# Performance work log

Measured on AMD Instinct MI355X. Metric: run time of the kernel, lower is better.

The kernel has to match this reference:

```python
import jax, jax.numpy as jnp
import numpy as np

B, L, D_IN, D = 64, 512, 1024, 1024


def setup_inputs() -> dict:
    key = jax.random.key(0)
    k1, k2, k3, k4, k5 = jax.random.split(key, 5)
    x = jax.random.normal(k1, (B, L, D_IN), dtype=jnp.float32)
    Wk = jax.random.normal(k2, (D_IN, 3 * D), dtype=jnp.float32) * (1.0 / np.sqrt(D_IN))
    Wr = jax.random.normal(k3, (D, 3 * D), dtype=jnp.float32) * (1.0 / np.sqrt(D))
    c0 = jax.random.normal(k4, (B, D), dtype=jnp.float32)
    h0 = jax.random.normal(k5, (B, D), dtype=jnp.float32)
    return {"x": x, "Wk": Wk, "Wr": Wr, "c0": c0, "h0": h0}


def reference(x, Wk, Wr, c0, h0):
    # Precompute input projection as one large GEMM: [B,L,3D]
    x_proj = jnp.einsum("bli,ig->blg", x, Wk)

    def step(carry, xp_t):
        c, h = carry  # c: long-term memory [B,D], h: previous output [B,D]
        gates = xp_t + h @ Wr  # [B,3D]
        f, o, g = jnp.split(gates, 3, axis=-1)
        sf = jax.nn.sigmoid(f)
        c_new = c * sf + (1.0 - sf) * jnp.tanh(g)
        h_new = jax.nn.sigmoid(o) * jnp.tanh(c_new)
        return (c_new, h_new), h_new

    # scan over time: move L to leading axis
    _, hs = jax.lax.scan(step, (c0, h0), jnp.swapaxes(x_proj, 0, 1))
    return jnp.swapaxes(hs, 0, 1)  # [B,L,D]
```

## Files before the change

### kernel.cpp

```cpp
#include <hip/hip_runtime.h>


typedef float    f32x4 __attribute__((ext_vector_type(4)));
typedef _Float16 half8 __attribute__((ext_vector_type(8)));
typedef _Float16 half4 __attribute__((ext_vector_type(4)));

#define AS1 __attribute__((address_space(1)))
#define AS3 __attribute__((address_space(3)))

#define B_  64
#define L_  512
#define D_  1024
#define N3_ 3072

#define WKT_OFF   0LL
#define WRT_OFF   6291456LL
#define XH_OFF    12582912LL
#define H16_OFF   79691776LL
#define BAR_OFF   79953920LL
#define XPROJ_OFF 79958016LL

__device__ __forceinline__ float sigmoidf_fast(float x) {
  return __builtin_amdgcn_rcpf(1.f + __builtin_amdgcn_exp2f(-1.4426950408889634f * x));
}
__device__ __forceinline__ float tanhf_fast(float x) {
  return 1.f - 2.f * __builtin_amdgcn_rcpf(1.f + __builtin_amdgcn_exp2f(2.8853900817779268f * x));
}

#define ALOAD(dst, addr) \
  asm volatile("global_load_dwordx4 %0, %1, off" : "=v"(dst) : "v"(addr))
#define VMCNT0() asm volatile("s_waitcnt vmcnt(0)" ::: "memory")

__device__ __forceinline__ void gload_lds16(const void* g, void* l) {
  __builtin_amdgcn_global_load_lds((const AS1 unsigned int*)g,
                                   (AS3 unsigned int*)l, 16, 0, 0);
}

__global__ void zero_bar(unsigned* __restrict__ bar) {
  bar[blockIdx.x * 256 + threadIdx.x] = 0u;
}

__global__ __launch_bounds__(256) void transpose_f16(
    const float* __restrict__ Wk, const float* __restrict__ Wr,
    _Float16* __restrict__ WkT, _Float16* __restrict__ WrT)
{
  __shared__ float tile[32][33];
  int b = blockIdx.x;
  const float* in = Wk; _Float16* outp = WkT;
  if (b >= 3072) { b -= 3072; in = Wr; outp = WrT; }
  const int n0 = (b % 96) * 32;
  const int k0 = (b / 96) * 32;
  const int tx = threadIdx.x & 31, ty = threadIdx.x >> 5;
#pragma unroll
  for (int i = 0; i < 32; i += 8)
    tile[ty + i][tx] = in[(size_t)(k0 + ty + i) * N3_ + n0 + tx];
  __syncthreads();
#pragma unroll
  for (int i = 0; i < 32; i += 8)
    outp[(size_t)(n0 + ty + i) * D_ + k0 + tx] = (_Float16)tile[tx][ty + i];
}

__global__ void convert_inputs(const f32x4* __restrict__ x, const f32x4* __restrict__ h0,
                               half4* __restrict__ xh, half4* __restrict__ h16a,
                               half4* __restrict__ h16b)
{
  const int NX = (B_ * L_ * D_) / 4;
  const int NH = (B_ * D_) / 4;
  for (int i = blockIdx.x * blockDim.x + threadIdx.x; i < NX + NH;
       i += gridDim.x * blockDim.x) {
    if (i < NX) {
      xh[i] = __builtin_convertvector(x[i], half4);
    } else {
      half4 v = __builtin_convertvector(h0[i - NX], half4);
      h16a[i - NX] = v;
      h16b[i - NX] = v;
    }
  }
}

__global__ __launch_bounds__(256) void gemm_xproj(
    const _Float16* __restrict__ A,
    const _Float16* __restrict__ BT,
    _Float16* __restrict__ C)
{
  __shared__ _Float16 As[128 * 32];
  __shared__ _Float16 Bs[128 * 32];
  const int tid = threadIdx.x, wave = tid >> 6, lane = tid & 63;
  const int mt = blockIdx.x / 24, ntile = blockIdx.x % 24;
  const int m0 = mt * 128, n0 = ntile * 128;
  const int l15 = lane & 15, l4h = lane >> 4;
  const int wm = (wave >> 1) * 64, wn = (wave & 1) * 64;

  const int c0i = wave * 2;
  const int lrow = lane >> 2;
  const int skel = 8 * ((lane & 3) ^ (lrow & 3));

  f32x4 acc[4][4];
#pragma unroll
  for (int i = 0; i < 4; ++i)
#pragma unroll
    for (int j = 0; j < 4; ++j) { f32x4 z = {0.f,0.f,0.f,0.f}; acc[i][j] = z; }

  for (int kk = 0; kk < 32; ++kk) {
    __syncthreads();
#pragma unroll
    for (int i = 0; i < 2; ++i) {
      const int c = c0i + i;
      const int row = c * 16 + lrow;
      gload_lds16(A  + (((size_t)(m0 + row)) << 10) + (kk << 5) + skel, &As[c << 9]);
      gload_lds16(BT + (((size_t)(n0 + row)) << 10) + (kk << 5) + skel, &Bs[c << 9]);
    }
    __syncthreads();
    half8 af[4], bf[4];
#pragma unroll
    for (int i = 0; i < 4; ++i) {
      const int ar = wm + i * 16 + l15;
      af[i] = *(const half8*)&As[(ar << 5) + ((l4h ^ (ar & 3)) << 3)];
      const int br = wn + i * 16 + l15;
      bf[i] = *(const half8*)&Bs[(br << 5) + ((l4h ^ (br & 3)) << 3)];
    }
#pragma unroll
    for (int i = 0; i < 4; ++i)
#pragma unroll
      for (int j = 0; j < 4; ++j)
        acc[i][j] = __builtin_amdgcn_mfma_f32_16x16x32_f16(af[i], bf[j], acc[i][j], 0, 0, 0);
  }
#pragma unroll
  for (int i = 0; i < 4; ++i) {
    const int row = m0 + wm + i * 16 + l4h * 4;
#pragma unroll
    for (int j = 0; j < 4; ++j) {
      const int col = n0 + wn + j * 16 + l15;
      _Float16* cp = C + (size_t)row * N3_ + col;
#pragma unroll
      for (int r = 0; r < 4; ++r)
        __builtin_nontemporal_store((_Float16)acc[i][j][r], cp + (size_t)r * N3_);
    }
  }
}

__global__ __launch_bounds__(256, 1) void lstm_scan(
    const _Float16* __restrict__ WrT,
    const _Float16* __restrict__ xproj,
    const float*    __restrict__ c0,
    float*          __restrict__ out,
    _Float16*       __restrict__ h16,
    unsigned*       __restrict__ bar)
{
  const int tid = threadIdx.x, wave = tid >> 6, lane = tid & 63;
  const int bid = blockIdx.x;
  const int grp = bid & 3;
  const int ord = bid >> 2;
  const int b0 = grp * 16;
  const int d0 = ord * 32;
  const int l15 = lane & 15, l4h = lane >> 4;
  const int kbase = wave * 256;

  unsigned* const gbase = bar + grp * 256;
  unsigned* const leafp = gbase + (ord & 3) * 16;

  half8 Wrf[2][3][8];
#pragma unroll
  for (int nt = 0; nt < 2; ++nt)
#pragma unroll
    for (int g = 0; g < 3; ++g) {
      const _Float16* rr = WrT + (size_t)(g * D_ + d0 + nt * 16 + l15) * D_ + kbase + l4h * 8;
#pragma unroll
      for (int kt = 0; kt < 8; ++kt) ALOAD(Wrf[nt][g][kt], rr + kt * 32);
    }
  VMCNT0();

  const int rb = tid >> 4;
  const int rd16 = tid & 15;
  float c_0 = c0[(size_t)(b0 + rb) * D_ + d0 + rd16];
  float c_1 = c0[(size_t)(b0 + rb) * D_ + d0 + 16 + rd16];

  __shared__ float part[4][2][48][20];
  __shared__ float obuf[16][512];

  const size_t hoff    = (size_t)(b0 + l15) * D_ + kbase + l4h * 8;
  const size_t outidx0 = ((size_t)(b0 + rb) * L_) * D_ + d0 + rd16;
  const size_t hidx0   = (size_t)(b0 + rb) * D_ + d0 + rd16;
  const _Float16* xpbase = xproj + ((size_t)(b0 + rb) * L_) * N3_ + d0 + rd16;

  _Float16* hc = h16;
  _Float16* hn = h16 + B_ * D_;

  float xf0 = (float)xpbase[0],  xo0 = (float)xpbase[D_],      xg0 = (float)xpbase[2 * D_];
  float xf1 = (float)xpbase[16], xo1 = (float)xpbase[D_ + 16], xg1 = (float)xpbase[2 * D_ + 16];

  for (int t = 0; t < L_; ++t) {
    half8 af[8];
    const _Float16* hrow = hc + hoff;
#pragma unroll
    for (int kt = 0; kt < 8; ++kt) af[kt] = *(const half8*)(hrow + kt * 32);

    f32x4 acc[2][3];
#pragma unroll
    for (int nt = 0; nt < 2; ++nt)
#pragma unroll
      for (int g = 0; g < 3; ++g) { f32x4 z = {0.f,0.f,0.f,0.f}; acc[nt][g] = z; }
#pragma unroll
    for (int kt = 0; kt < 8; ++kt)
#pragma unroll
      for (int nt = 0; nt < 2; ++nt)
#pragma unroll
        for (int g = 0; g < 3; ++g)
          acc[nt][g] = __builtin_amdgcn_mfma_f32_16x16x32_f16(af[kt], Wrf[nt][g][kt], acc[nt][g], 0, 0, 0);

#pragma unroll
    for (int nt = 0; nt < 2; ++nt)
#pragma unroll
      for (int g = 0; g < 3; ++g)
        *(f32x4*)&part[wave][nt][g * 16 + l15][l4h * 4] = acc[nt][g];
    __syncthreads();

    float fv0 = xf0, ov0 = xo0, gv0 = xg0;
    float fv1 = xf1, ov1 = xo1, gv1 = xg1;
#pragma unroll
    for (int w = 0; w < 4; ++w) {
      fv0 += part[w][0][rd16][rb];       fv1 += part[w][1][rd16][rb];
      ov0 += part[w][0][16 + rd16][rb];  ov1 += part[w][1][16 + rd16][rb];
      gv0 += part[w][0][32 + rd16][rb];  gv1 += part[w][1][32 + rd16][rb];
    }
    const float sf0 = sigmoidf_fast(fv0), sf1 = sigmoidf_fast(fv1);
    c_0 = c_0 * sf0 + (1.f - sf0) * tanhf_fast(gv0);
    c_1 = c_1 * sf1 + (1.f - sf1) * tanhf_fast(gv1);
    const float h0v = sigmoidf_fast(ov0) * tanhf_fast(c_0);
    const float h1v = sigmoidf_fast(ov1) * tanhf_fast(c_1);

    hn[hidx0]      = (_Float16)h0v;
    hn[hidx0 + 16] = (_Float16)h1v;
    obuf[t & 15][tid]       = h0v;
    obuf[t & 15][tid + 256] = h1v;

    __syncthreads();
    if (tid == 0)
      __hip_atomic_fetch_add(leafp, 1u, __ATOMIC_ACQ_REL, __HIP_MEMORY_SCOPE_AGENT);

    if ((t & 15) == 15) {
      float* op0 = out + outidx0 + (size_t)(t - 15) * D_;
#pragma unroll
      for (int j = 0; j < 16; ++j) {
        __builtin_nontemporal_store(obuf[j][tid],       op0 + (size_t)j * D_);
        __builtin_nontemporal_store(obuf[j][tid + 256], op0 + (size_t)j * D_ + 16);
      }
    }
    if (t + 1 < L_) {
      const _Float16* xp = xpbase + (size_t)(t + 1) * N3_;
      xf0 = (float)xp[0];   xo0 = (float)xp[D_];        xg0 = (float)xp[2 * D_];
      xf1 = (float)xp[16];  xo1 = (float)xp[D_ + 16];   xg1 = (float)xp[2 * D_ + 16];
    }
    __builtin_amdgcn_sched_barrier(0);

    if (tid == 0) {
      const unsigned tgt = 8u * (unsigned)(t + 1);
      while (true) {
        bool ok = true;
#pragma unroll
        for (int i = 0; i < 4; ++i)
          ok = ok & (__hip_atomic_load(gbase + i * 16, __ATOMIC_RELAXED,
                                       __HIP_MEMORY_SCOPE_AGENT) >= tgt);
        if (ok) break;
        __builtin_amdgcn_s_sleep(1);
      }
      __builtin_amdgcn_fence(__ATOMIC_ACQUIRE, "agent");
    }
    __syncthreads();

    _Float16* tmp = hc; hc = hn; hn = tmp;
  }
}

extern "C" void kernel_launch(void* const* d_in, const int* in_sizes, int n_in,
                              void* d_out, int out_size, void* d_ws, size_t ws_size,
                              hipStream_t stream) {
  const float* x  = (const float*)d_in[0];
  const float* Wk = (const float*)d_in[1];
  const float* Wr = (const float*)d_in[2];
  const float* c0 = (const float*)d_in[3];
  const float* h0 = (const float*)d_in[4];
  float* out = (float*)d_out;

  char* ws = (char*)d_ws;
  _Float16* WkT   = (_Float16*)(ws + WKT_OFF);
  _Float16* WrT   = (_Float16*)(ws + WRT_OFF);
  _Float16* xh    = (_Float16*)(ws + XH_OFF);
  _Float16* h16   = (_Float16*)(ws + H16_OFF);
  unsigned* bar   = (unsigned*)(ws + BAR_OFF);
  _Float16* xproj = (_Float16*)(ws + XPROJ_OFF);

  hipLaunchKernelGGL(zero_bar, dim3(4), dim3(256), 0, stream, bar);
  hipLaunchKernelGGL(transpose_f16, dim3(6144), dim3(256), 0, stream,
                     Wk, Wr, WkT, WrT);
  hipLaunchKernelGGL(convert_inputs, dim3(2048), dim3(256), 0, stream,
                     (const f32x4*)x, (const f32x4*)h0,
                     (half4*)xh, (half4*)h16, (half4*)(h16 + B_ * D_));
  hipLaunchKernelGGL(gemm_xproj, dim3(6144), dim3(256), 0, stream,
                     xh, WkT, xproj);

  void* kargs[6] = {(void*)&WrT, (void*)&xproj, (void*)&c0,
                    (void*)&out, (void*)&h16, (void*)&bar};
  hipLaunchCooperativeKernel((void*)lstm_scan, dim3(128), dim3(256), kargs, 0, stream);
}
```

Baseline: 3.762 ms.

## Halve scan grid to 64 blocks of 512 threads, drop output staging buffer

The recurrent scan kernel now launches 64 cooperative blocks of 8 waves instead of 128 blocks of 4 waves. Each block covers 64 hidden columns, with two column-halves of 4 K-split waves each, and the barrier target is lowered to match. The shared-memory output staging buffer is removed and each step's h is stored directly to global memory. The aim is to halve the number of blocks taking part in each per-timestep grid barrier, at the cost of larger blocks and more scattered per-step output stores.

Measured after the change: 3.664 ms. 2.6% less time.

```diff
diff --git a/kernel.cpp b/kernel.cpp
--- a/kernel.cpp
+++ b/kernel.cpp
@@ -139,7 +139,7 @@
   }
 }
 
-__global__ __launch_bounds__(256, 1) void lstm_scan(
+__global__ __launch_bounds__(512, 2) void lstm_scan(
     const _Float16* __restrict__ WrT,
     const _Float16* __restrict__ xproj,
     const float*    __restrict__ c0,
@@ -152,9 +152,10 @@
   const int grp = bid & 3;
   const int ord = bid >> 2;
   const int b0 = grp * 16;
-  const int d0 = ord * 32;
+  const int d0 = ord * 64;
   const int l15 = lane & 15, l4h = lane >> 4;
-  const int kbase = wave * 256;
+  const int ks = wave & 3, ch = wave >> 2;
+  const int kbase = ks * 256;
 
   unsigned* const gbase = bar + grp * 256;
   unsigned* const leafp = gbase + (ord & 3) * 16;
@@ -164,30 +165,36 @@
   for (int nt = 0; nt < 2; ++nt)
 #pragma unroll
     for (int g = 0; g < 3; ++g) {
-      const _Float16* rr = WrT + (size_t)(g * D_ + d0 + nt * 16 + l15) * D_ + kbase + l4h * 8;
+      const _Float16* rr = WrT +
+          (size_t)(g * D_ + d0 + ch * 32 + nt * 16 + l15) * D_ + kbase + l4h * 8;
 #pragma unroll
       for (int kt = 0; kt < 8; ++kt) ALOAD(Wrf[nt][g][kt], rr + kt * 32);
     }
   VMCNT0();
 
-  const int rb = tid >> 4;
-  const int rd16 = tid & 15;
-  float c_0 = c0[(size_t)(b0 + rb) * D_ + d0 + rd16];
-  float c_1 = c0[(size_t)(b0 + rb) * D_ + d0 + 16 + rd16];
-
-  __shared__ float part[4][2][48][20];
-  __shared__ float obuf[16][512];
+  const int rb = tid >> 5;
+  const int c  = tid & 31;
+  const int ntc = c >> 4, rd16 = c & 15;
+  float cc[2];
+  cc[0] = c0[(size_t)(b0 + rb) * D_ + d0 + c];
+  cc[1] = c0[(size_t)(b0 + rb) * D_ + d0 + 32 + c];
+
+  __shared__ float part[4][4][48][20];
 
   const size_t hoff    = (size_t)(b0 + l15) * D_ + kbase + l4h * 8;
-  const size_t outidx0 = ((size_t)(b0 + rb) * L_) * D_ + d0 + rd16;
-  const size_t hidx0   = (size_t)(b0 + rb) * D_ + d0 + rd16;
-  const _Float16* xpbase = xproj + ((size_t)(b0 + rb) * L_) * N3_ + d0 + rd16;
+  const size_t outidx0 = ((size_t)(b0 + rb) * L_) * D_ + d0 + c;
+  const size_t hidx0   = (size_t)(b0 + rb) * D_ + d0 + c;
+  const _Float16* xpbase = xproj + ((size_t)(b0 + rb) * L_) * N3_ + d0 + c;
 
   _Float16* hc = h16;
   _Float16* hn = h16 + B_ * D_;
 
-  float xf0 = (float)xpbase[0],  xo0 = (float)xpbase[D_],      xg0 = (float)xpbase[2 * D_];
-  float xf1 = (float)xpbase[16], xo1 = (float)xpbase[D_ + 16], xg1 = (float)xpbase[2 * D_ + 16];
+  float xpv[3][2];
+#pragma unroll
+  for (int g = 0; g < 3; ++g) {
+    xpv[g][0] = (float)xpbase[(size_t)g * D_];
+    xpv[g][1] = (float)xpbase[(size_t)g * D_ + 32];
+  }
 
   for (int t = 0; t < L_; ++t) {
     half8 af[8];
@@ -212,49 +219,49 @@
     for (int nt = 0; nt < 2; ++nt)
 #pragma unroll
       for (int g = 0; g < 3; ++g)
-        *(f32x4*)&part[wave][nt][g * 16 + l15][l4h * 4] = acc[nt][g];
-    __syncthreads();
-
-    float fv0 = xf0, ov0 = xo0, gv0 = xg0;
-    float fv1 = xf1, ov1 = xo1, gv1 = xg1;
-#pragma unroll
-    for (int w = 0; w < 4; ++w) {
-      fv0 += part[w][0][rd16][rb];       fv1 += part[w][1][rd16][rb];
-      ov0 += part[w][0][16 + rd16][rb];  ov1 += part[w][1][16 + rd16][rb];
-      gv0 += part[w][0][32 + rd16][rb];  gv1 += part[w][1][32 + rd16][rb];
-    }
-    const float sf0 = sigmoidf_fast(fv0), sf1 = sigmoidf_fast(fv1);
-    c_0 = c_0 * sf0 + (1.f - sf0) * tanhf_fast(gv0);
-    c_1 = c_1 * sf1 + (1.f - sf1) * tanhf_fast(gv1);
-    const float h0v = sigmoidf_fast(ov0) * tanhf_fast(c_0);
-    const float h1v = sigmoidf_fast(ov1) * tanhf_fast(c_1);
-
-    hn[hidx0]      = (_Float16)h0v;
-    hn[hidx0 + 16] = (_Float16)h1v;
-    obuf[t & 15][tid]       = h0v;
-    obuf[t & 15][tid + 256] = h1v;
+        *(f32x4*)&part[ks][ch * 2 + nt][g * 16 + l15][l4h * 4] = acc[nt][g];
+    __syncthreads();
+
+    float hv[2];
+#pragma unroll
+    for (int H = 0; H < 2; ++H) {
+      const int e = H * 2 + ntc;
+      float fv = xpv[0][H], ov = xpv[1][H], gv = xpv[2][H];
+#pragma unroll
+      for (int k = 0; k < 4; ++k) {
+        fv += part[k][e][rd16][rb];
+        ov += part[k][e][16 + rd16][rb];
+        gv += part[k][e][32 + rd16][rb];
+      }
+      const float sf = sigmoidf_fast(fv);
+      cc[H] = cc[H] * sf + (1.f - sf) * tanhf_fast(gv);
+      hv[H] = sigmoidf_fast(ov) * tanhf_fast(cc[H]);
+    }
+
+    hn[hidx0]      = (_Float16)hv[0];
+    hn[hidx0 + 32] = (_Float16)hv[1];
 
     __syncthreads();
     if (tid == 0)
       __hip_atomic_fetch_add(leafp, 1u, __ATOMIC_ACQ_REL, __HIP_MEMORY_SCOPE_AGENT);
 
-    if ((t & 15) == 15) {
-      float* op0 = out + outidx0 + (size_t)(t - 15) * D_;
-#pragma unroll
-      for (int j = 0; j < 16; ++j) {
-        __builtin_nontemporal_store(obuf[j][tid],       op0 + (size_t)j * D_);
-        __builtin_nontemporal_store(obuf[j][tid + 256], op0 + (size_t)j * D_ + 16);
-      }
+    {
+      float* op = out + outidx0 + (size_t)t * D_;
+      __builtin_nontemporal_store(hv[0], op);
+      __builtin_nontemporal_store(hv[1], op + 32);
     }
     if (t + 1 < L_) {
       const _Float16* xp = xpbase + (size_t)(t + 1) * N3_;
-      xf0 = (float)xp[0];   xo0 = (float)xp[D_];        xg0 = (float)xp[2 * D_];
-      xf1 = (float)xp[16];  xo1 = (float)xp[D_ + 16];   xg1 = (float)xp[2 * D_ + 16];
+#pragma unroll
+      for (int g = 0; g < 3; ++g) {
+        xpv[g][0] = (float)xp[(size_t)g * D_];
+        xpv[g][1] = (float)xp[(size_t)g * D_ + 32];
+      }
     }
     __builtin_amdgcn_sched_barrier(0);
 
     if (tid == 0) {
-      const unsigned tgt = 8u * (unsigned)(t + 1);
+      const unsigned tgt = 4u * (unsigned)(t + 1);
       while (true) {
         bool ok = true;
 #pragma unroll
@@ -301,5 +308,5 @@
 
   void* kargs[6] = {(void*)&WrT, (void*)&xproj, (void*)&c0,
                     (void*)&out, (void*)&h16, (void*)&bar};
-  hipLaunchCooperativeKernel((void*)lstm_scan, dim3(128), dim3(256), kargs, 0, stream);
-}
+  hipLaunchCooperativeKernel((void*)lstm_scan, dim3(64), dim3(512), kargs, 0, stream);
+}
```
